# Performance work log

Measured on AMD Instinct MI355X. Metric: run time of the kernel, lower is better.

## Reference

```python
import jax, jax.numpy as jnp
import numpy as np

# module hyperparameters (init_kwargs)
WEIGHT = 2e-9
SIGMA_RGB = 0.15   # images in [0,1]; equals canonical 15/255
SIGMA_XY = 100.0
SCALE = 0.5

N, C, K, H, W = 4, 3, 21, 128, 128


def _nearest(x, oh, ow):
    """torch F.interpolate(mode='nearest'): src = floor(dst * in/out)."""
    h, w = x.shape[-2], x.shape[-1]
    iy = jnp.floor(jnp.arange(oh) * (h / oh)).astype(jnp.int32)
    ix = jnp.floor(jnp.arange(ow) * (w / ow)).astype(jnp.int32)
    return x[..., iy[:, None], ix[None, :]]


def _bilinear(x, oh, ow):
    """torch F.interpolate(mode='bilinear', align_corners=False)."""
    h, w = x.shape[-2], x.shape[-1]

    def coords(o, s):
        c = (jnp.arange(o, dtype=jnp.float32) + 0.5) * (s / o) - 0.5
        c = jnp.clip(c, 0.0, s - 1.0)
        c0 = jnp.floor(c).astype(jnp.int32)
        c1 = jnp.minimum(c0 + 1, s - 1)
        return c0, c1, c - c0

    y0, y1, wy = coords(oh, h)
    x0, x1, wx = coords(ow, w)
    wy = wy[:, None]
    wx = wx[None, :]
    v00 = x[..., y0[:, None], x0[None, :]]
    v01 = x[..., y0[:, None], x1[None, :]]
    v10 = x[..., y1[:, None], x0[None, :]]
    v11 = x[..., y1[:, None], x1[None, :]]
    top = v00 * (1.0 - wx) + v01 * wx
    bot = v10 * (1.0 - wx) + v11 * wx
    return top * (1.0 - wy) + bot * wy


def setup_inputs() -> dict:
    key = jax.random.key(0)
    k1, k2 = jax.random.split(key)
    images = jax.random.uniform(k1, (N, C, H, W), jnp.float32)
    segmentations = jax.random.uniform(k2, (N, K, H, W), jnp.float32)
    ROIs = jnp.ones((N, H, W), jnp.float32)
    return {"images": images, "segmentations": segmentations, "ROIs": ROIs}


def reference(images, segmentations, ROIs):
    oh, ow = int(H * SCALE), int(W * SCALE)
    img_s = _nearest(images, oh, ow)           # [N,3,oh,ow]
    seg_s = _bilinear(segmentations, oh, ow)   # [N,K,oh,ow]
    roi_s = _nearest(ROIs, oh, ow)             # [N,oh,ow]
    seg_m = seg_s * roi_s[:, None]             # seg * ROI (per class)
    sxy = SIGMA_XY * SCALE

    # exact dense Gaussian bilateral kernel that the permutohedral lattice
    # (bilateralfilter_batch) approximates: k(i,j) = exp(-|p_i-p_j|^2/(2 sxy^2)
    #                                                  -|I_i-I_j|^2/(2 srgb^2))
    yy, xx = jnp.meshgrid(jnp.arange(oh, dtype=jnp.float32),
                          jnp.arange(ow, dtype=jnp.float32), indexing="ij")
    pos = jnp.stack([xx, yy], 0) / sxy         # [2,oh,ow]

    def per_image(img, seg):
        feat = jnp.concatenate([pos, img / SIGMA_RGB], 0).reshape(5, -1).T  # [P,5]
        sq = jnp.sum(feat * feat, axis=-1)                                  # [P]
        d2 = jnp.maximum(sq[:, None] + sq[None, :] - 2.0 * (feat @ feat.T), 0.0)
        Wk = jnp.exp(-0.5 * d2)                                             # [P,P]
        s = seg.reshape(K, -1)                                              # [K,P]
        AS = s @ Wk                                                         # filtered seg
        return jnp.sum(s * AS)

    vals = jax.vmap(per_image)(img_s, seg_m)   # [N]
    loss = -(jnp.sum(vals)) / N                # densecrf_loss
    return WEIGHT * loss
```

## Files before the change

kernel.cpp:

```cpp
#include <hip/hip_runtime.h>

#define NIMG 4
#define CCH  3
#define KCH  21
#define HIN  128
#define WIN  128
#define OH   64
#define OW   64
#define PPX  (OH*OW)

#define PRE2 1.20112241f

#define SEGW  24
#define FEATW 8

#define BLOCK  256
#define JCHUNK 256
#define IBLK   64

#define NSLOT  64

typedef _Float16 half_t;
typedef half_t half8  __attribute__((ext_vector_type(8)));
typedef float  f32x4v __attribute__((ext_vector_type(4)));

#define FEATH_OFF ((size_t)NIMG*PPX*SEGW*2)
#define SQF_OFF   (FEATH_OFF + (size_t)NIMG*PPX*FEATW*2)
#define SLOT_OFF  (SQF_OFF + (size_t)NIMG*PPX*4)

__global__ __launch_bounds__(BLOCK) void crf_prep(const float* __restrict__ img,
                                                  const float* __restrict__ seg,
                                                  const float* __restrict__ roi,
                                                  half_t* __restrict__ segH,
                                                  half_t* __restrict__ featH,
                                                  float* __restrict__ sqF,
                                                  float* __restrict__ slots) {
    int g = blockIdx.x * BLOCK + threadIdx.x;
    if (g < NSLOT) slots[g * 16] = 0.0f;
    int q  = g & 31;
    int pl = g >> 5;
    int n  = pl >> 12;
    int p  = pl & (PPX - 1);
    int y = p >> 6, x = p & 63;
    int y2 = 2 * y, x2 = 2 * x;

    if (q < SEGW) {
        float v = 0.0f;
        if (q < KCH) {
            const float* s0 = seg + (((size_t)n * KCH + q) * HIN + y2) * WIN + x2;
            float r = roi[((size_t)n * HIN + y2) * WIN + x2];
            v = 0.25f * (s0[0] + s0[1] + s0[WIN] + s0[WIN + 1]) * r;
        }
        segH[(size_t)pl * SEGW + q] = (half_t)v;
    } else if (q == 24) {
        float fx = (float)x * (PRE2 / 50.0f);
        float fy = (float)y * (PRE2 / 50.0f);
        const size_t ib = (((size_t)n * CCH) * HIN + y2) * WIN + x2;
        float fr = img[ib]                         * (PRE2 / 0.15f);
        float fg = img[ib + (size_t)HIN * WIN]     * (PRE2 / 0.15f);
        float fb = img[ib + 2 * (size_t)HIN * WIN] * (PRE2 / 0.15f);
        half_t h0 = (half_t)fx, h1 = (half_t)fy, h2 = (half_t)fr,
               h3 = (half_t)fg, h4 = (half_t)fb;
        half8 fh = {h0, h1, h2, h3, h4, (half_t)0, (half_t)0, (half_t)0};
        *(half8*)(featH + (size_t)pl * FEATW) = fh;
        float a0 = (float)h0, a1 = (float)h1, a2 = (float)h2,
              a3 = (float)h3, a4 = (float)h4;
        sqF[pl] = 0.5f * (a0 * a0 + a1 * a1 + a2 * a2 + a3 * a3 + a4 * a4);
    }
}

__global__ __launch_bounds__(BLOCK) void crf_main(const half_t* __restrict__ segH,
                                                  const half_t* __restrict__ featH,
                                                  const float* __restrict__ sqF,
                                                  float* __restrict__ slots) {
    const int bx = blockIdx.x;
    const int n  = blockIdx.y;

    int g = 0;
#pragma unroll
    for (int t = 1; t < 16; ++t) {
        int off = 64 * t - 2 * t * (t - 1);
        if (bx >= off) g = t;
    }
    int rem = bx - (64 * g - 2 * g * (g - 1));
    int c   = 16 - g;
    int iq  = (rem >= c) + (rem >= 2 * c) + (rem >= 3 * c);
    int I   = 4 * g + iq;
    int J   = g + (rem - iq * c);
    const bool diag = (J == (I >> 2));

    const half_t* segN  = segH  + (size_t)n * PPX * SEGW;
    const half_t* featN = featH + (size_t)n * PPX * FEATW;
    const float*  sqN   = sqF   + (size_t)n * PPX;

    __shared__ alignas(16) half_t segJ[JCHUNK * SEGW];
    __shared__ alignas(16) half_t featJ[JCHUNK * FEATW];
    __shared__ alignas(16) half_t zrow[8];
    __shared__ float hJ[JCHUNK];
    __shared__ float wsum[BLOCK / 64];

    const int tid  = threadIdx.x;
    const int lane = tid & 63, wv = tid >> 6;
    const int m = lane & 15, quad = lane >> 4;
    const int i0 = I * IBLK + wv * 16;
    const int j0 = J * JCHUNK;
    const int kq = (quad < 2) ? quad : 2;

    half8 hz = {};

    half8 aseg  = *(const half8*)(segN  + (size_t)(i0 + m) * SEGW + kq * 8);
    half8 afeat = *(const half8*)(featN + (size_t)(i0 + m) * FEATW);
    f32x4v hi   = *(const f32x4v*)(sqN + i0 + quad * 4);
    if (quad == 3) aseg  = hz;
    if (quad != 0) afeat = hz;
    f32x4v nh = -hi;

    {
        const f32x4v* gsrc = (const f32x4v*)(segN + (size_t)j0 * SEGW);
        f32x4v* ldst = (f32x4v*)segJ;
#pragma unroll
        for (int v = 0; v < 3; ++v) ldst[tid + v * BLOCK] = gsrc[tid + v * BLOCK];
        ((f32x4v*)featJ)[tid] = ((const f32x4v*)(featN + (size_t)j0 * FEATW))[tid];
        hJ[tid] = sqN[j0 + tid];
        if (tid < 8) zrow[tid] = (half_t)0;
    }
    __syncthreads();

    const half_t* bsp; int bstep;
    if (quad == 3) { bsp = zrow;                       bstep = 0; }
    else           { bsp = segJ + m * SEGW + quad * 8; bstep = 16 * SEGW; }
    const half_t* bfp; int fstep;
    if (quad == 0) { bfp = featJ + m * FEATW;          fstep = 16 * FEATW; }
    else           { bfp = zrow;                       fstep = 0; }

    float racc = 0.0f;
    const f32x4v zero4 = {0.0f, 0.0f, 0.0f, 0.0f};

#pragma unroll 4
    for (int jt = 0; jt < JCHUNK / 16; ++jt) {
        half8 bseg = *(const half8*)bsp;  bsp += bstep;
        half8 bft  = *(const half8*)bfp;  bfp += fstep;
        float hc = hJ[jt * 16 + m];

        f32x4v c4 = {nh[0] - hc, nh[1] - hc, nh[2] - hc, nh[3] - hc};
        f32x4v E  = __builtin_amdgcn_mfma_f32_16x16x32_f16(afeat, bft, c4, 0, 0, 0);
        f32x4v Gs = __builtin_amdgcn_mfma_f32_16x16x32_f16(aseg, bseg, zero4, 0, 0, 0);

        if (!diag) {
#pragma unroll
            for (int r = 0; r < 4; ++r)
                racc = fmaf(__builtin_amdgcn_exp2f(E[r]), Gs[r], racc);
        } else {
            const int jg = j0 + jt * 16 + m;
#pragma unroll
            for (int r = 0; r < 4; ++r) {
                int ig = i0 + quad * 4 + r;
                float sel = (jg > ig) ? 1.0f : ((jg == ig) ? 0.0f : -100000.0f);
                racc = fmaf(__builtin_amdgcn_exp2f(E[r] + sel), Gs[r], racc);
            }
        }
    }

#pragma unroll
    for (int off = 32; off > 0; off >>= 1) racc += __shfl_down(racc, off);
    if (lane == 0) wsum[wv] = racc;
    __syncthreads();
    if (tid == 0) {
        float s = wsum[0] + wsum[1] + wsum[2] + wsum[3];
        if (!diag) s *= 2.0f;
        int slot = (bx + 544 * n) & (NSLOT - 1);
        atomicAdd(&slots[slot * 16], s);
    }
}

__global__ __launch_bounds__(64) void crf_final(const float* __restrict__ slots,
                                                float* __restrict__ out) {
    int lane = threadIdx.x;
    float v = slots[lane * 16];
#pragma unroll
    for (int off = 32; off > 0; off >>= 1) v += __shfl_down(v, off);
    if (lane == 0) out[0] = v * (-5.0e-10f);
}

extern "C" void kernel_launch(void* const* d_in, const int* in_sizes, int n_in,
                              void* d_out, int out_size, void* d_ws, size_t ws_size,
                              hipStream_t stream) {
    const float* img = (const float*)d_in[0];
    const float* seg = (const float*)d_in[1];
    const float* roi = (const float*)d_in[2];
    float* out = (float*)d_out;

    char* wsb = (char*)d_ws;
    half_t* segH  = (half_t*)(wsb);
    half_t* featH = (half_t*)(wsb + FEATH_OFF);
    float*  sqF   = (float*)(wsb + SQF_OFF);
    float*  slots = (float*)(wsb + SLOT_OFF);

    crf_prep<<<(NIMG * PPX * 32) / BLOCK, BLOCK, 0, stream>>>(img, seg, roi,
                                                              segH, featH, sqF, slots);

    dim3 grid(544, NIMG);
    crf_main<<<grid, BLOCK, 0, stream>>>(segH, featH, sqF, slots);

    crf_final<<<1, 64, 0, stream>>>(slots, out);
}
```

Baseline: 77.75 us.

## Fuse final reduction into main kernel via last-block counter; remap prep threads

Removes the separate final-reduction launch. Each main-kernel block now bumps a global counter after adding its partial sum, and whichever block arrives last reads the slots and writes the output. The prep kernel's thread mapping changes so that the channel index is the high part of the thread id. Adjacent threads now handle adjacent pixels of one channel, which changes the memory access pattern. Prep also resets the counter. This saves one kernel launch at the cost of an extra atomic and a fence in every block.

After: 106.0 us. 1.36x slower.

```diff
diff --git a/kernel.cpp b/kernel.cpp
--- a/kernel.cpp
+++ b/kernel.cpp
@@ -8,6 +8,7 @@
 #define OH   64
 #define OW   64
 #define PPX  (OH*OW)
+#define NPIX (NIMG*PPX)
 
 #define PRE2 1.20112241f
 
@@ -19,14 +20,16 @@
 #define IBLK   64
 
 #define NSLOT  64
+#define NBLK_MAIN (544*NIMG)
 
 typedef _Float16 half_t;
 typedef half_t half8  __attribute__((ext_vector_type(8)));
 typedef float  f32x4v __attribute__((ext_vector_type(4)));
 
-#define FEATH_OFF ((size_t)NIMG*PPX*SEGW*2)
-#define SQF_OFF   (FEATH_OFF + (size_t)NIMG*PPX*FEATW*2)
-#define SLOT_OFF  (SQF_OFF + (size_t)NIMG*PPX*4)
+#define FEATH_OFF ((size_t)NPIX*SEGW*2)
+#define SQF_OFF   (FEATH_OFF + (size_t)NPIX*FEATW*2)
+#define SLOT_OFF  (SQF_OFF + (size_t)NPIX*4)
+#define CNT_OFF   (SLOT_OFF + (size_t)NSLOT*16*4)
 
 __global__ __launch_bounds__(BLOCK) void crf_prep(const float* __restrict__ img,
                                                   const float* __restrict__ seg,
@@ -34,11 +37,11 @@
                                                   half_t* __restrict__ segH,
                                                   half_t* __restrict__ featH,
                                                   float* __restrict__ sqF,
-                                                  float* __restrict__ slots) {
-    int g = blockIdx.x * BLOCK + threadIdx.x;
-    if (g < NSLOT) slots[g * 16] = 0.0f;
-    int q  = g & 31;
-    int pl = g >> 5;
+                                                  float* __restrict__ slots,
+                                                  unsigned* __restrict__ counter) {
+    int g  = blockIdx.x * BLOCK + threadIdx.x;
+    int q  = g >> 14;
+    int pl = g & (NPIX - 1);
     int n  = pl >> 12;
     int p  = pl & (PPX - 1);
     int y = p >> 6, x = p & 63;
@@ -66,13 +69,18 @@
         float a0 = (float)h0, a1 = (float)h1, a2 = (float)h2,
               a3 = (float)h3, a4 = (float)h4;
         sqF[pl] = 0.5f * (a0 * a0 + a1 * a1 + a2 * a2 + a3 * a3 + a4 * a4);
+    } else if (q == 25) {
+        if (pl < NSLOT) slots[pl * 16] = 0.0f;
+        if (pl == NSLOT) *counter = 0u;
     }
 }
 
 __global__ __launch_bounds__(BLOCK) void crf_main(const half_t* __restrict__ segH,
                                                   const half_t* __restrict__ featH,
                                                   const float* __restrict__ sqF,
-                                                  float* __restrict__ slots) {
+                                                  float* __restrict__ slots,
+                                                  unsigned* __restrict__ counter,
+                                                  float* __restrict__ out) {
     const int bx = blockIdx.x;
     const int n  = blockIdx.y;
 
@@ -98,6 +106,7 @@
     __shared__ alignas(16) half_t zrow[8];
     __shared__ float hJ[JCHUNK];
     __shared__ float wsum[BLOCK / 64];
+    __shared__ int   lastFlag;
 
     const int tid  = threadIdx.x;
     const int lane = tid & 63, wv = tid >> 6;
@@ -170,16 +179,19 @@
         if (!diag) s *= 2.0f;
         int slot = (bx + 544 * n) & (NSLOT - 1);
         atomicAdd(&slots[slot * 16], s);
-    }
-}
-
-__global__ __launch_bounds__(64) void crf_final(const float* __restrict__ slots,
-                                                float* __restrict__ out) {
-    int lane = threadIdx.x;
-    float v = slots[lane * 16];
-#pragma unroll
-    for (int off = 32; off > 0; off >>= 1) v += __shfl_down(v, off);
-    if (lane == 0) out[0] = v * (-5.0e-10f);
+        __threadfence();
+        unsigned old = atomicAdd(counter, 1u);
+        lastFlag = (old == NBLK_MAIN - 1) ? 1 : 0;
+    }
+    __syncthreads();
+
+    if (lastFlag && wv == 0) {
+        float v = __hip_atomic_load(&slots[lane * 16], __ATOMIC_RELAXED,
+                                    __HIP_MEMORY_SCOPE_AGENT);
+#pragma unroll
+        for (int off = 32; off > 0; off >>= 1) v += __shfl_down(v, off);
+        if (lane == 0) out[0] = v * (-5.0e-10f);
+    }
 }
 
 extern "C" void kernel_launch(void* const* d_in, const int* in_sizes, int n_in,
@@ -195,12 +207,11 @@
     half_t* featH = (half_t*)(wsb + FEATH_OFF);
     float*  sqF   = (float*)(wsb + SQF_OFF);
     float*  slots = (float*)(wsb + SLOT_OFF);
-
-    crf_prep<<<(NIMG * PPX * 32) / BLOCK, BLOCK, 0, stream>>>(img, seg, roi,
-                                                              segH, featH, sqF, slots);
+    unsigned* cnt = (unsigned*)(wsb + CNT_OFF);
+
+    crf_prep<<<(NPIX * 32) / BLOCK, BLOCK, 0, stream>>>(img, seg, roi,
+                                                        segH, featH, sqF, slots, cnt);
 
     dim3 grid(544, NIMG);
-    crf_main<<<grid, BLOCK, 0, stream>>>(segH, featH, sqF, slots);
-
-    crf_final<<<1, 64, 0, stream>>>(slots, out);
+    crf_main<<<grid, BLOCK, 0, stream>>>(segH, featH, sqF, slots, cnt, out);
 }
```
